# Performance work log

Hardware: AMD Instinct MI355X
Metric: run time of the kernel (lower is better)

The kernel has to match this reference:

```python
import jax, jax.numpy as jnp
import numpy as np

N_NODES = 50000
N_EDGES = 800000
HIDDEN = 128
OUT = 128


def setup_inputs() -> dict:
    key = jax.random.key(0)
    k1, k2, k3, k4, k5, k6 = jax.random.split(key, 6)
    h = jax.random.normal(k1, (N_NODES, HIDDEN), dtype=jnp.float32)
    src = jax.random.randint(k2, (N_EDGES,), 0, N_NODES, dtype=jnp.int64)
    dst = jax.random.randint(k3, (N_EDGES,), 0, N_NODES, dtype=jnp.int64)
    scale = 1.0 / np.sqrt(HIDDEN)
    W_edge = jax.random.normal(k4, (OUT, HIDDEN), dtype=jnp.float32) * scale
    W_self = jax.random.normal(k5, (OUT, HIDDEN), dtype=jnp.float32) * scale
    b_self = jax.random.normal(k6, (OUT,), dtype=jnp.float32) * scale
    return {"h": h, "src": src, "dst": dst, "W_edge": W_edge, "W_self": W_self, "b_self": b_self}


def reference(h, src, dst, W_edge, W_self, b_self):
    n = h.shape[0]
    # edge_transform(src_features): same linear on every edge -> transform nodes once, then gather
    msg_node = h @ W_edge.T                       # [N, OUT]
    msg = msg_node[src]                           # [E, OUT] gather
    sums = jax.ops.segment_sum(msg, dst, num_segments=n)  # [N, OUT] scatter-add
    deg = jax.ops.segment_sum(jnp.ones((dst.shape[0],), dtype=h.dtype), dst, num_segments=n)
    h1 = sums / jnp.maximum(deg, 1.0)[:, None]    # mean; zero in-degree -> 0 (DGL semantics)
    out = jax.nn.relu(h @ W_self.T + b_self + h1)
    return out
```

## Files before the change

kernel.cpp:

```cpp
#include <hip/hip_runtime.h>

#define N_HID 128
#define CAP   32
#define OVF_CAP 8192
#define NSLICE 8
#define PBLK   256

typedef short bf16x8 __attribute__((ext_vector_type(8)));
typedef float f32x4  __attribute__((ext_vector_type(4)));

static __device__ __forceinline__ unsigned short f2bf(float f)
{
    unsigned int u = __float_as_uint(f);
    u = (u + 0x7fffu + ((u >> 16) & 1u)) >> 16;
    return (unsigned short)u;
}
static __device__ __forceinline__ unsigned int pack2(float a, float b)
{
    return (unsigned int)f2bf(a) | ((unsigned int)f2bf(b) << 16);
}
static __device__ __forceinline__ float lo_f(unsigned int x)
{
    return __uint_as_float(x << 16);
}
static __device__ __forceinline__ float hi_f(unsigned int x)
{
    return __uint_as_float(x & 0xffff0000u);
}
static __device__ __forceinline__ int slice_of(int d, float sln)
{
    int sl = (int)((float)d * sln);
    return sl > NSLICE - 1 ? NSLICE - 1 : sl;
}

__global__ __launch_bounds__(256) void count_fragw_cast(
    const int* __restrict__ dst, int* __restrict__ blockCnt,
    int* __restrict__ cnt, int* __restrict__ ovfn, int E, int n, float sln,
    const float* __restrict__ We, const float* __restrict__ Ws,
    unsigned short* __restrict__ Be, unsigned short* __restrict__ Bs,
    const float* __restrict__ h, unsigned short* __restrict__ hbf, int total,
    unsigned int* __restrict__ bucket32, unsigned int sent2)
{
    int t = threadIdx.x, b = blockIdx.x;

    if (b >= PBLK + 16) {
        int idx = (b - PBLK - 16) * 2048 + t * 8;
        if (idx + 8 <= total) {
            float4 v0 = *(const float4*)&h[idx];
            float4 v1 = *(const float4*)&h[idx + 4];
            uint4 pk;
            pk.x = pack2(v0.x, v0.y);
            pk.y = pack2(v0.z, v0.w);
            pk.z = pack2(v1.x, v1.y);
            pk.w = pack2(v1.z, v1.w);
            *(uint4*)&hbf[idx] = pk;
        } else if (idx + 8 <= total + N_HID) {
            uint4 z = {0u, 0u, 0u, 0u};
            *(uint4*)&hbf[idx] = z;
        }
        return;
    }

    if (b >= PBLK) {
        int bb = b - PBLK;
        const float* srcw = (bb < 8) ? We : Ws;
        unsigned short* dstF = (bb < 8) ? Be : Bs;
        int rt = bb & 7;
        int kc = t >> 6, l = t & 63, m = l & 15, q = l >> 4;
        const float* p = &srcw[(size_t)(rt * 16 + m) * N_HID + kc * 32 + q * 8];
        float4 v0 = *(const float4*)p;
        float4 v1 = *(const float4*)(p + 4);
        uint4 pk;
        pk.x = pack2(v0.x, v0.y);
        pk.y = pack2(v0.z, v0.w);
        pk.z = pack2(v1.x, v1.y);
        pk.w = pack2(v1.z, v1.w);
        *(uint4*)&dstF[(size_t)rt * 2048 + kc * 512 + l * 8] = pk;
        return;
    }

    for (int i = b * 256 + t; i < n; i += PBLK * 256) cnt[i] = 0;
    {
        const int nb32 = n * (CAP / 2);
        for (int i = b * 256 + t; i < nb32; i += PBLK * 256) bucket32[i] = sent2;
    }
    if (b == 0 && t == 0) *ovfn = 0;

    int c[NSLICE];
#pragma unroll
    for (int s = 0; s < NSLICE; ++s) c[s] = 0;

    for (int e = b * 256 + t; e < E; e += PBLK * 256) {
        int sl = slice_of(dst[e], sln);
#pragma unroll
        for (int s = 0; s < NSLICE; ++s) c[s] += (sl == s);
    }

    __shared__ int red[NSLICE * 4];
    int lane = t & 63, wid = t >> 6;
#pragma unroll
    for (int s = 0; s < NSLICE; ++s) {
        int v = c[s];
#pragma unroll
        for (int off = 32; off; off >>= 1) v += __shfl_down(v, off);
        if (lane == 0) red[s * 4 + wid] = v;
    }
    __syncthreads();
    if (t < NSLICE)
        blockCnt[t * PBLK + b] = red[t*4+0] + red[t*4+1] + red[t*4+2] + red[t*4+3];
}

__global__ __launch_bounds__(256) void part_scan_scatter(
    const int* __restrict__ blockCnt,
    int* __restrict__ sbase,
    const int* __restrict__ src, const int* __restrict__ dst,
    unsigned int* __restrict__ part,
    int E, int n, float sln)
{
    __shared__ int wsm[4];
    __shared__ int lbase[PBLK * NSLICE];
    __shared__ int cur[NSLICE];
    int t = threadIdx.x, lane = t & 63, wid = t >> 6;
    int v[8]; int s = 0;
#pragma unroll
    for (int i = 0; i < 8; ++i) { v[i] = blockCnt[t * 8 + i]; s += v[i]; }
    int val = s;
#pragma unroll
    for (int off = 1; off < 64; off <<= 1) {
        int y = __shfl_up(val, off);
        if (lane >= off) val += y;
    }
    if (lane == 63) wsm[wid] = val;
    __syncthreads();
    if (t == 0) { int a = 0; for (int w = 0; w < 4; ++w) { int tmp = wsm[w]; wsm[w] = a; a += tmp; } }
    __syncthreads();
    int excl = wsm[wid] + val - s;
#pragma unroll
    for (int i = 0; i < 8; ++i) { int tv = v[i]; lbase[t * 8 + i] = excl; excl += tv; }
    __syncthreads();

    const int b = blockIdx.x;
    if (t < NSLICE) cur[t] = lbase[t * PBLK + b];
    if (b == 0) {
        if (t < NSLICE) sbase[t] = lbase[t * PBLK];
        if (t == 0)     sbase[NSLICE] = E;
    }
    __syncthreads();

    for (int e = b * 256 + t; e < E; e += PBLK * 256) {
        int d = dst[e], sv = src[e];
        int sl  = slice_of(d, sln);
        int pos = atomicAdd(&cur[sl], 1);
        part[pos] = ((unsigned int)d << 16) | (unsigned int)sv;
    }
}

__global__ __launch_bounds__(256) void bucket_scatter2(
    const unsigned int* __restrict__ part,
    const int* __restrict__ sbase,
    int* __restrict__ cnt,
    unsigned short* __restrict__ bucket,
    int* __restrict__ ovfn,
    long long* __restrict__ ovf)
{
    const int slice = blockIdx.x & 7;
    const int g     = blockIdx.x >> 3;
    const int nG    = (int)(gridDim.x >> 3);
    const int lo    = sbase[slice];
    const int hi    = sbase[slice + 1];
    const int m     = hi - lo;

    const int chunk = (m + nG - 1) / nG;
    const int e0 = lo + g * chunk;
    int e1 = e0 + chunk; if (e1 > hi) e1 = hi;

    for (int e = e0 + (int)threadIdx.x; e < e1; e += 256) {
        unsigned int pk = part[e];
        int d = (int)(pk >> 16);
        int s = (int)(pk & 0xffffu);
        int c = atomicAdd(&cnt[d], 1);
        if (c < CAP) {
            bucket[(size_t)d * CAP + c] = (unsigned short)s;
        } else {
            int o = atomicAdd(ovfn, 1);
            if (o < OVF_CAP) ovf[o] = ((long long)d << 32) | (unsigned int)s;
        }
    }
}

__global__ __launch_bounds__(256) void gather_gemm(
    const int* __restrict__ cnt,
    const unsigned short* __restrict__ bucket,
    const int* __restrict__ ovfn,
    const long long* __restrict__ ovf,
    const unsigned short* __restrict__ hbf,
    const unsigned short* __restrict__ Be,
    const unsigned short* __restrict__ Bsf,
    const float* __restrict__ bias,
    float* __restrict__ out,
    int n, int nrt)
{
    __shared__ __align__(16) unsigned int wl[16 * 68];

    const int t    = threadIdx.x;
    const int lane = t & 63;
    const int widu = __builtin_amdgcn_readfirstlane(t >> 6);
    const int slice = blockIdx.x & 7;
    const int g     = blockIdx.x >> 3;
    const int tLo = (int)(((long long)slice * nrt) >> 3);
    const int tHi = (int)(((long long)(slice + 1) * nrt) >> 3);
    const int tile = tLo + g;
    if (tile >= tHi) return;

    const unsigned int* h32 = (const unsigned int*)hbf;

#pragma unroll
    for (int k = 0; k < 4; ++k) {
        const int mm   = widu * 4 + k;
        const int node = tile * 16 + mm;
        float ax = 0.f, ay = 0.f;
        int deg = 0;
        if (node < n) {
            deg = cnt[node];
            const unsigned short* bk = &bucket[(size_t)node * CAP];

            {
                unsigned int v[16];
#pragma unroll
                for (int i = 0; i < 16; ++i) {
                    const unsigned int r = bk[i];
                    v[i] = h32[(size_t)r * 64 + lane];
                }
#pragma unroll
                for (int i = 0; i < 16; ++i) {
                    ax += lo_f(v[i]); ay += hi_f(v[i]);
                }
            }
            if (deg > 16) {
                unsigned int v[16];
#pragma unroll
                for (int i = 0; i < 16; ++i) {
                    const unsigned int r = bk[16 + i];
                    v[i] = h32[(size_t)r * 64 + lane];
                }
#pragma unroll
                for (int i = 0; i < 16; ++i) {
                    ax += lo_f(v[i]); ay += hi_f(v[i]);
                }
            }

            if (deg > CAP) {
                int no = *ovfn; if (no > OVF_CAP) no = OVF_CAP;
                for (int o = 0; o < no; ++o) {
                    long long pk = ovf[o];
                    if ((int)(pk >> 32) == node) {
                        unsigned int x = h32[(size_t)(unsigned int)pk * 64 + lane];
                        ax += lo_f(x); ay += hi_f(x);
                    }
                }
            }
        }

        float sc = deg > 0 ? 1.0f / (float)deg : 0.f;
        wl[mm * 68 + lane] = pack2(ax * sc, ay * sc);
    }
    __syncthreads();

    const int rr = lane & 15, qq = lane >> 4;
    const int row0 = tile * 16;

    bf16x8 ah[4], ag[4];
#pragma unroll
    for (int kc = 0; kc < 4; ++kc) {
        int gr = row0 + rr; if (gr > n - 1) gr = n - 1;
        ah[kc] = *(const bf16x8*)&hbf[(size_t)gr * N_HID + kc * 32 + qq * 8];
        ag[kc] = *(const bf16x8*)&wl[rr * 68 + kc * 16 + qq * 4];
    }

    const int colb = lane & 15;
    const int rq   = (lane >> 4) * 4;

#pragma unroll
    for (int cti = 0; cti < 2; ++cti) {
        int ct = widu * 2 + cti;
        const bf16x8* BpS = (const bf16x8*)(Bsf + (size_t)ct * 2048);
        const bf16x8* BpE = (const bf16x8*)(Be  + (size_t)ct * 2048);
        f32x4 acc = {0.f, 0.f, 0.f, 0.f};
        acc = __builtin_amdgcn_mfma_f32_16x16x32_bf16(ah[0], BpS[lane],       acc, 0, 0, 0);
        acc = __builtin_amdgcn_mfma_f32_16x16x32_bf16(ah[1], BpS[64 + lane],  acc, 0, 0, 0);
        acc = __builtin_amdgcn_mfma_f32_16x16x32_bf16(ah[2], BpS[128 + lane], acc, 0, 0, 0);
        acc = __builtin_amdgcn_mfma_f32_16x16x32_bf16(ah[3], BpS[192 + lane], acc, 0, 0, 0);
        acc = __builtin_amdgcn_mfma_f32_16x16x32_bf16(ag[0], BpE[lane],       acc, 0, 0, 0);
        acc = __builtin_amdgcn_mfma_f32_16x16x32_bf16(ag[1], BpE[64 + lane],  acc, 0, 0, 0);
        acc = __builtin_amdgcn_mfma_f32_16x16x32_bf16(ag[2], BpE[128 + lane], acc, 0, 0, 0);
        acc = __builtin_amdgcn_mfma_f32_16x16x32_bf16(ag[3], BpE[192 + lane], acc, 0, 0, 0);

        int col = ct * 16 + colb;
        float bv = bias[col];
#pragma unroll
        for (int r = 0; r < 4; ++r) {
            int row = row0 + rq + r;
            if (row < n) out[(size_t)row * N_HID + col] = fmaxf(acc[r] + bv, 0.f);
        }
    }
}

extern "C" void kernel_launch(void* const* d_in, const int* in_sizes, int n_in,
                              void* d_out, int out_size, void* d_ws, size_t ws_size,
                              hipStream_t stream)
{
    const float* h   = (const float*)d_in[0];
    const int*   src = (const int*)d_in[1];
    const int*   dst = (const int*)d_in[2];
    const float* We  = (const float*)d_in[3];
    const float* Ws  = (const float*)d_in[4];
    const float* bs  = (const float*)d_in[5];
    float*       out = (float*)d_out;

    const int n   = in_sizes[0] / N_HID;
    const int E   = in_sizes[1];
    const int nrt = (n + 15) / 16;
    const float sln = (float)NSLICE / (float)n;
    const int total = n * N_HID;

    unsigned short* hbf  = (unsigned short*)d_ws;
    unsigned short* bucket = hbf + (size_t)(n + 1) * N_HID;
    unsigned short* Be  = bucket + (size_t)n * CAP;
    unsigned short* Bs  = Be + 8 * 2048;
    int*  cnt  = (int*)(Bs + 8 * 2048);
    int*  ovfn = cnt + n;
    long long* ovf = (long long*)(ovfn + 8);
    int*  blockCnt  = (int*)(ovf + OVF_CAP);
    int*  sbase     = blockCnt + PBLK * NSLICE;
    unsigned int* part = (unsigned int*)(sbase + 16);

    const unsigned int sent2 = (unsigned int)n | ((unsigned int)n << 16);
    const int castBlocks = (total + N_HID + 2047) / 2048;

    const int maxTilesPerSlice = (nrt + NSLICE - 1) / NSLICE;
    const int ggGrid = NSLICE * maxTilesPerSlice;

    count_fragw_cast<<<PBLK + 16 + castBlocks, 256, 0, stream>>>(
        dst, blockCnt, cnt, ovfn, E, n, sln, We, Ws, Be, Bs, h, hbf, total,
        (unsigned int*)bucket, sent2);
    part_scan_scatter<<<PBLK, 256, 0, stream>>>(blockCnt, sbase, src, dst,
                                                part, E, n, sln);
    bucket_scatter2<<<2048, 256, 0, stream>>>(part, sbase, cnt, bucket, ovfn, ovf);
    gather_gemm<<<ggGrid, 256, 0, stream>>>(cnt, bucket, ovfn, ovf,
                                            hbf, Be, Bs, bs, out, n, nrt);
}
```

Measured before the change: 171.5 us.

## Drop slice partitioning pass and scatter edges directly into per-node buckets

Removes the per-slice counting, prefix scan and partition scatter that first grouped edges by destination slice before bucketing. Edges are now read straight from src/dst and atomically appended to per-destination buckets, which saves one kernel launch plus a full write and read of the partitioned edge array. The cost is that bucket atomics and writes become randomly spread across all nodes rather than localized per slice, which may hurt L2 locality.

```diff
diff --git a/kernel.cpp b/kernel.cpp
--- a/kernel.cpp
+++ b/kernel.cpp
@@ -27,15 +27,9 @@
 {
     return __uint_as_float(x & 0xffff0000u);
 }
-static __device__ __forceinline__ int slice_of(int d, float sln)
-{
-    int sl = (int)((float)d * sln);
-    return sl > NSLICE - 1 ? NSLICE - 1 : sl;
-}
-
-__global__ __launch_bounds__(256) void count_fragw_cast(
-    const int* __restrict__ dst, int* __restrict__ blockCnt,
-    int* __restrict__ cnt, int* __restrict__ ovfn, int E, int n, float sln,
+
+__global__ __launch_bounds__(256) void fill_fragw_cast(
+    int* __restrict__ cnt, int* __restrict__ ovfn, int n,
     const float* __restrict__ We, const float* __restrict__ Ws,
     unsigned short* __restrict__ Be, unsigned short* __restrict__ Bs,
     const float* __restrict__ h, unsigned short* __restrict__ hbf, int total,
@@ -85,99 +79,20 @@
         for (int i = b * 256 + t; i < nb32; i += PBLK * 256) bucket32[i] = sent2;
     }
     if (b == 0 && t == 0) *ovfn = 0;
-
-    int c[NSLICE];
-#pragma unroll
-    for (int s = 0; s < NSLICE; ++s) c[s] = 0;
-
-    for (int e = b * 256 + t; e < E; e += PBLK * 256) {
-        int sl = slice_of(dst[e], sln);
-#pragma unroll
-        for (int s = 0; s < NSLICE; ++s) c[s] += (sl == s);
-    }
-
-    __shared__ int red[NSLICE * 4];
-    int lane = t & 63, wid = t >> 6;
-#pragma unroll
-    for (int s = 0; s < NSLICE; ++s) {
-        int v = c[s];
-#pragma unroll
-        for (int off = 32; off; off >>= 1) v += __shfl_down(v, off);
-        if (lane == 0) red[s * 4 + wid] = v;
-    }
-    __syncthreads();
-    if (t < NSLICE)
-        blockCnt[t * PBLK + b] = red[t*4+0] + red[t*4+1] + red[t*4+2] + red[t*4+3];
-}
-
-__global__ __launch_bounds__(256) void part_scan_scatter(
-    const int* __restrict__ blockCnt,
-    int* __restrict__ sbase,
+}
+
+__global__ __launch_bounds__(256) void bucket_scatter_direct(
     const int* __restrict__ src, const int* __restrict__ dst,
-    unsigned int* __restrict__ part,
-    int E, int n, float sln)
-{
-    __shared__ int wsm[4];
-    __shared__ int lbase[PBLK * NSLICE];
-    __shared__ int cur[NSLICE];
-    int t = threadIdx.x, lane = t & 63, wid = t >> 6;
-    int v[8]; int s = 0;
-#pragma unroll
-    for (int i = 0; i < 8; ++i) { v[i] = blockCnt[t * 8 + i]; s += v[i]; }
-    int val = s;
-#pragma unroll
-    for (int off = 1; off < 64; off <<= 1) {
-        int y = __shfl_up(val, off);
-        if (lane >= off) val += y;
-    }
-    if (lane == 63) wsm[wid] = val;
-    __syncthreads();
-    if (t == 0) { int a = 0; for (int w = 0; w < 4; ++w) { int tmp = wsm[w]; wsm[w] = a; a += tmp; } }
-    __syncthreads();
-    int excl = wsm[wid] + val - s;
-#pragma unroll
-    for (int i = 0; i < 8; ++i) { int tv = v[i]; lbase[t * 8 + i] = excl; excl += tv; }
-    __syncthreads();
-
-    const int b = blockIdx.x;
-    if (t < NSLICE) cur[t] = lbase[t * PBLK + b];
-    if (b == 0) {
-        if (t < NSLICE) sbase[t] = lbase[t * PBLK];
-        if (t == 0)     sbase[NSLICE] = E;
-    }
-    __syncthreads();
-
-    for (int e = b * 256 + t; e < E; e += PBLK * 256) {
-        int d = dst[e], sv = src[e];
-        int sl  = slice_of(d, sln);
-        int pos = atomicAdd(&cur[sl], 1);
-        part[pos] = ((unsigned int)d << 16) | (unsigned int)sv;
-    }
-}
-
-__global__ __launch_bounds__(256) void bucket_scatter2(
-    const unsigned int* __restrict__ part,
-    const int* __restrict__ sbase,
     int* __restrict__ cnt,
     unsigned short* __restrict__ bucket,
     int* __restrict__ ovfn,
-    long long* __restrict__ ovf)
-{
-    const int slice = blockIdx.x & 7;
-    const int g     = blockIdx.x >> 3;
-    const int nG    = (int)(gridDim.x >> 3);
-    const int lo    = sbase[slice];
-    const int hi    = sbase[slice + 1];
-    const int m     = hi - lo;
-
-    const int chunk = (m + nG - 1) / nG;
-    const int e0 = lo + g * chunk;
-    int e1 = e0 + chunk; if (e1 > hi) e1 = hi;
-
-    for (int e = e0 + (int)threadIdx.x; e < e1; e += 256) {
-        unsigned int pk = part[e];
-        int d = (int)(pk >> 16);
-        int s = (int)(pk & 0xffffu);
+    long long* __restrict__ ovf,
+    int E)
+{
+    const int stride = (int)(gridDim.x * 256);
+    for (int e = (int)(blockIdx.x * 256 + threadIdx.x); e < E; e += stride) {
+        int d = dst[e];
+        int s = src[e];
         int c = atomicAdd(&cnt[d], 1);
         if (c < CAP) {
             bucket[(size_t)d * CAP + c] = (unsigned short)s;
@@ -320,7 +235,6 @@
     const int n   = in_sizes[0] / N_HID;
     const int E   = in_sizes[1];
     const int nrt = (n + 15) / 16;
-    const float sln = (float)NSLICE / (float)n;
     const int total = n * N_HID;
 
     unsigned short* hbf  = (unsigned short*)d_ws;
@@ -330,9 +244,6 @@
     int*  cnt  = (int*)(Bs + 8 * 2048);
     int*  ovfn = cnt + n;
     long long* ovf = (long long*)(ovfn + 8);
-    int*  blockCnt  = (int*)(ovf + OVF_CAP);
-    int*  sbase     = blockCnt + PBLK * NSLICE;
-    unsigned int* part = (unsigned int*)(sbase + 16);
 
     const unsigned int sent2 = (unsigned int)n | ((unsigned int)n << 16);
     const int castBlocks = (total + N_HID + 2047) / 2048;
@@ -340,12 +251,11 @@
     const int maxTilesPerSlice = (nrt + NSLICE - 1) / NSLICE;
     const int ggGrid = NSLICE * maxTilesPerSlice;
 
-    count_fragw_cast<<<PBLK + 16 + castBlocks, 256, 0, stream>>>(
-        dst, blockCnt, cnt, ovfn, E, n, sln, We, Ws, Be, Bs, h, hbf, total,
+    fill_fragw_cast<<<PBLK + 16 + castBlocks, 256, 0, stream>>>(
+        cnt, ovfn, n, We, Ws, Be, Bs, h, hbf, total,
         (unsigned int*)bucket, sent2);
-    part_scan_scatter<<<PBLK, 256, 0, stream>>>(blockCnt, sbase, src, dst,
-                                                part, E, n, sln);
-    bucket_scatter2<<<2048, 256, 0, stream>>>(part, sbase, cnt, bucket, ovfn, ovf);
+    bucket_scatter_direct<<<2048, 256, 0, stream>>>(src, dst, cnt, bucket,
+                                                    ovfn, ovf, E);
     gather_gemm<<<ggGrid, 256, 0, stream>>>(cnt, bucket, ovfn, ovf,
                                             hbf, Be, Bs, bs, out, n, nrt);
 }
```

Measured after the change: 185.5 us. +8.2%, slower.
